# Kernel optimization log

Measured on AMD Instinct MI355X. Metric: run time of the kernel, lower is better.

Reference implementation:

```python
import jax, jax.numpy as jnp
import numpy as np

BS, NS, S = 4, 16384, 8
C_PLANE, RES = 64, 128
IN_DIM = 3 * C_PLANE  # 192


def _bilerp(plane, uv):
    """plane: [B,C,H,W]; uv: [B,n,2] in [0,1] -> [B,n,C] bilinear samples (border clamp)."""
    B, C, H, W = plane.shape
    x = jnp.clip(uv[..., 0], 0.0, 1.0) * (W - 1)
    y = jnp.clip(uv[..., 1], 0.0, 1.0) * (H - 1)
    x0 = jnp.floor(x).astype(jnp.int32)
    y0 = jnp.floor(y).astype(jnp.int32)
    x1 = jnp.minimum(x0 + 1, W - 1)
    y1 = jnp.minimum(y0 + 1, H - 1)
    wx = (x - x0)[:, :, None]
    wy = (y - y0)[:, :, None]
    gat = jax.vmap(lambda p, yy, xx: p[:, yy, xx].T)  # per-batch gather -> [n,C]
    f00 = gat(plane, y0, x0)
    f01 = gat(plane, y0, x1)
    f10 = gat(plane, y1, x0)
    f11 = gat(plane, y1, x1)
    return (f00 * (1 - wx) * (1 - wy) + f01 * wx * (1 - wy)
            + f10 * (1 - wx) * wy + f11 * wx * wy)


def _sample_triplane(p, feat_xz, feat_xy, feat_yz):
    """p: [B,n,3] -> concat of bilinear samples from the three planes: [B,n,3C]."""
    f_xz = _bilerp(feat_xz, p[..., jnp.array([0, 2])])
    f_xy = _bilerp(feat_xy, p[..., jnp.array([0, 1])])
    f_yz = _bilerp(feat_yz, p[..., jnp.array([1, 2])])
    return jnp.concatenate([f_xz, f_xy, f_yz], axis=-1)


def setup_inputs() -> dict:
    key = jax.random.key(0)
    ks = jax.random.split(key, 12)
    w = 0.05  # small init so predicted offsets stay near the query point
    return {
        "query_pos": jax.random.uniform(ks[0], (BS, NS, 3), dtype=jnp.float32),
        "feat_xz": jax.random.normal(ks[1], (BS, C_PLANE, RES, RES), dtype=jnp.float32),
        "feat_xy": jax.random.normal(ks[2], (BS, C_PLANE, RES, RES), dtype=jnp.float32),
        "feat_yz": jax.random.normal(ks[3], (BS, C_PLANE, RES, RES), dtype=jnp.float32),
        "W_v": jax.random.normal(ks[4], (IN_DIM, IN_DIM), dtype=jnp.float32) * w,
        "b_v": jnp.zeros((IN_DIM,), jnp.float32),
        "W_out": jax.random.normal(ks[5], (IN_DIM, IN_DIM), dtype=jnp.float32) * w,
        "b_out": jnp.zeros((IN_DIM,), jnp.float32),
        "W_off": jax.random.normal(ks[6], (3 * S, IN_DIM), dtype=jnp.float32) * w,
        "b_off": jnp.zeros((3 * S,), jnp.float32),
        "W_wt": jax.random.normal(ks[7], (S, IN_DIM), dtype=jnp.float32) * w,
        "b_wt": jnp.zeros((S,), jnp.float32),
    }


def reference(query_pos, feat_xz, feat_xy, feat_yz, W_v, b_v, W_out, b_out,
              W_off, b_off, W_wt, b_wt):
    bs, ns, _ = query_pos.shape
    # feature at query points: [bs, ns, IN_DIM]
    feature = _sample_triplane(query_pos, feat_xz, feat_xy, feat_yz)
    # predicted per-sample offsets and weights
    off = (feature @ W_off.T + b_off).reshape(bs, ns, S, 3)
    wt = (feature @ W_wt.T + b_wt)[..., None]            # [bs, ns, S, 1]
    pts = off + query_pos[:, :, None, :]                  # [bs, ns, S, 3]
    # gather features at offset locations: [bs, ns*S, IN_DIM]
    aux = _sample_triplane(pts.reshape(bs, ns * S, 3), feat_xz, feat_xy, feat_yz)
    v = (aux @ W_v.T + b_v).reshape(bs, ns, S, -1)        # [bs, ns, S, hidden]
    out = (v * wt).sum(axis=-2)                           # weighted sum over samples
    out = out @ W_out.T + b_out + feature                 # residual add
    return out  # [bs, ns, IN_DIM]
```

## Files before the change

kernel.cpp:

```cpp
#include <hip/hip_runtime.h>

#define BS 4
#define NS 16384
#define S_SAMP 8
#define CPL 64
#define RES 128
#define IN_DIM 192
#define NPTS (BS * NS)
#define PL_STRIDE (RES * RES * CPL)
#define PLANES_T_FLOATS (BS * 3 * PL_STRIDE)

__global__ __launch_bounds__(256) void transpose_planes(
    const float* __restrict__ xz, const float* __restrict__ xy,
    const float* __restrict__ yz, float* __restrict__ T) {
  __shared__ float tile[64][33];
  int blk = blockIdx.x;
  int xt = blk & 3;
  int y  = (blk >> 2) & 127;
  int pl = (blk >> 9) % 3;
  int b  = blk / 1536;
  const float* src = (pl == 0) ? xz : ((pl == 1) ? xy : yz);
  src += (size_t)b * CPL * RES * RES + (size_t)y * RES + xt * 32;
  int tid = threadIdx.x;
  int xl = tid & 31, c0 = tid >> 5;
#pragma unroll
  for (int r = 0; r < 8; ++r) {
    int c = c0 + (r << 3);
    tile[c][xl] = src[(size_t)c * RES * RES + xl];
  }
  __syncthreads();
  float* dst = T + ((size_t)(b * 3 + pl) * RES * RES + (size_t)y * RES + xt * 32) * CPL;
  int c2 = tid & 63, x0 = tid >> 6;
#pragma unroll
  for (int r = 0; r < 8; ++r) {
    int xl2 = x0 + (r << 2);
    dst[(size_t)xl2 * CPL + c2] = tile[c2][xl2];
  }
}

__global__ __launch_bounds__(192) void precompute_wc(
    const float* __restrict__ W_v, const float* __restrict__ b_v,
    const float* __restrict__ W_out, float* __restrict__ WcT,
    float* __restrict__ bc) {
  int j = threadIdx.x;
  int k = blockIdx.x;
  if (k < IN_DIM) {
    float acc = 0.f;
    for (int m = 0; m < IN_DIM; ++m)
      acc += W_out[j * IN_DIM + m] * W_v[m * IN_DIM + k];
    WcT[k * IN_DIM + j] = acc;
  } else {
    float acc = 0.f;
    for (int m = 0; m < IN_DIM; ++m)
      acc += W_out[j * IN_DIM + m] * b_v[m];
    bc[j] = acc;
  }
}

__device__ __forceinline__ float bilerp_s(const float* __restrict__ pb, float u,
                                          float v, int lane) {
  u = fminf(fmaxf(u, 0.f), 1.f) * 127.f;
  v = fminf(fmaxf(v, 0.f), 1.f) * 127.f;
  float xf = floorf(u), yf = floorf(v);
  float wx = u - xf, wy = v - yf;
  int x0 = __builtin_amdgcn_readfirstlane((int)xf);
  int y0 = __builtin_amdgcn_readfirstlane((int)yf);
  int dx = (x0 < 127) ? CPL : 0;
  int dy = (y0 < 127) ? RES * CPL : 0;
  const float* b00 = pb + (((y0 << 7) + x0) << 6);
  float f00 = b00[lane];
  float f01 = b00[dx + lane];
  float f10 = b00[dy + lane];
  float f11 = b00[dy + dx + lane];
  float fx0 = f00 + wx * (f01 - f00);
  float fx1 = f10 + wx * (f11 - f10);
  return fx0 + wy * (fx1 - fx0);
}

__global__ __launch_bounds__(256, 4) void fused_sample(
    const float* __restrict__ qpos, const float* __restrict__ planesT,
    const float* __restrict__ W_off, const float* __restrict__ b_off,
    const float* __restrict__ W_wt, const float* __restrict__ b_wt,
    float* __restrict__ waux, float* __restrict__ swtg,
    float* __restrict__ featg) {
  __shared__ float feat_lds[4][IN_DIM];
  __shared__ float offwt[4][32];
  int w = threadIdx.x >> 6, lane = threadIdx.x & 63;
  int p = (blockIdx.x << 2) + w;
  int b = p >> 14;
  float qx = qpos[p * 3 + 0], qy = qpos[p * 3 + 1], qz = qpos[p * 3 + 2];
  const float* Tb = planesT + (size_t)b * 3 * PL_STRIDE;

  float f0 = bilerp_s(Tb, qx, qz, lane);
  float f1 = bilerp_s(Tb + PL_STRIDE, qx, qy, lane);
  float f2 = bilerp_s(Tb + 2 * PL_STRIDE, qy, qz, lane);
  feat_lds[w][lane] = f0;
  feat_lds[w][64 + lane] = f1;
  feat_lds[w][128 + lane] = f2;
  __syncthreads();

  {
    int oj = lane & 31;
    const float* row = (oj < 24) ? (W_off + oj * IN_DIM)
                                 : (W_wt + (oj - 24) * IN_DIM);
    float bias = (oj < 24) ? b_off[oj] : b_wt[oj - 24];
    int k0 = (lane >> 5) * 96;
    const float4* r4 = (const float4*)(row + k0);
    float a0 = 0.f, a1 = 0.f, a2 = 0.f, a3 = 0.f;
#pragma unroll
    for (int k4 = 0; k4 < 24; ++k4) {
      float4 rv = r4[k4];
      a0 += rv.x * feat_lds[w][k0 + 4 * k4 + 0];
      a1 += rv.y * feat_lds[w][k0 + 4 * k4 + 1];
      a2 += rv.z * feat_lds[w][k0 + 4 * k4 + 2];
      a3 += rv.w * feat_lds[w][k0 + 4 * k4 + 3];
    }
    float acc = (a0 + a1) + (a2 + a3);
    acc += __shfl_xor(acc, 32);
    if (lane < 32) offwt[w][oj] = acc + bias;
  }
  __syncthreads();

  float wa0 = 0.f, wa1 = 0.f, wa2 = 0.f, swt = 0.f;
#pragma unroll 4
  for (int s = 0; s < S_SAMP; ++s) {
    float wt = offwt[w][24 + s];
    float px = qx + offwt[w][3 * s + 0];
    float py = qy + offwt[w][3 * s + 1];
    float pz = qz + offwt[w][3 * s + 2];
    wa0 += wt * bilerp_s(Tb, px, pz, lane);
    wa1 += wt * bilerp_s(Tb + PL_STRIDE, px, py, lane);
    wa2 += wt * bilerp_s(Tb + 2 * PL_STRIDE, py, pz, lane);
    swt += wt;
  }

  size_t o = (size_t)p * IN_DIM + lane;
  waux[o] = wa0; waux[o + 64] = wa1; waux[o + 128] = wa2;
  if (lane == 0) swtg[p] = swt;
  featg[o] = f0; featg[o + 64] = f1; featg[o + 128] = f2;
}

__global__ __launch_bounds__(512) void out_gemm(
    const float* __restrict__ waux, const float* __restrict__ swtg,
    const float* __restrict__ WcT, const float* __restrict__ bc,
    const float* __restrict__ b_out, float* __restrict__ out) {
  __shared__ float wtile[64 * IN_DIM];
  int tid = threadIdx.x;
  int w = tid >> 6, lane = tid & 63;
  int p0 = blockIdx.x * 128 + w * 16;

  float acc[4][4][3] = {};
  for (int c = 0; c < 3; ++c) {
#pragma unroll
    for (int r = 0; r < 24; ++r)
      wtile[tid + r * 512] = WcT[c * 64 * IN_DIM + tid + r * 512];
    __syncthreads();
#pragma unroll
    for (int g = 0; g < 4; ++g) {
      const float* wrow[4];
#pragma unroll
      for (int q = 0; q < 4; ++q)
        wrow[q] = waux +
                  (size_t)__builtin_amdgcn_readfirstlane(p0 + g * 4 + q) * IN_DIM +
                  c * 64;
#pragma unroll 4
      for (int k = 0; k < 64; ++k) {
        float v0 = wtile[k * IN_DIM + lane];
        float v1 = wtile[k * IN_DIM + 64 + lane];
        float v2 = wtile[k * IN_DIM + 128 + lane];
#pragma unroll
        for (int q = 0; q < 4; ++q) {
          float wv = wrow[q][k];
          acc[g][q][0] += v0 * wv;
          acc[g][q][1] += v1 * wv;
          acc[g][q][2] += v2 * wv;
        }
      }
    }
    __syncthreads();
  }
#pragma unroll
  for (int g = 0; g < 4; ++g)
#pragma unroll
    for (int q = 0; q < 4; ++q) {
      int p = p0 + g * 4 + q;
      float sw = swtg[p];
#pragma unroll
      for (int t = 0; t < 3; ++t) {
        int j = lane + t * 64;
        size_t o = (size_t)p * IN_DIM + j;
        out[o] = acc[g][q][t] + sw * bc[j] + b_out[j] + out[o];
      }
    }
}

extern "C" void kernel_launch(void* const* d_in, const int* in_sizes, int n_in,
                              void* d_out, int out_size, void* d_ws,
                              size_t ws_size, hipStream_t stream) {
  const float* qpos  = (const float*)d_in[0];
  const float* xz    = (const float*)d_in[1];
  const float* xy    = (const float*)d_in[2];
  const float* yz    = (const float*)d_in[3];
  const float* W_v   = (const float*)d_in[4];
  const float* b_v   = (const float*)d_in[5];
  const float* W_out = (const float*)d_in[6];
  const float* b_out = (const float*)d_in[7];
  const float* W_off = (const float*)d_in[8];
  const float* b_off = (const float*)d_in[9];
  const float* W_wt  = (const float*)d_in[10];
  const float* b_wt  = (const float*)d_in[11];

  float* ws      = (float*)d_ws;
  float* planesT = ws;
  float* waux    = planesT + PLANES_T_FLOATS;
  float* swtg    = waux + (size_t)NPTS * IN_DIM;
  float* WcT     = swtg + NPTS;
  float* bc      = WcT + IN_DIM * IN_DIM;
  float* out     = (float*)d_out;

  hipLaunchKernelGGL(transpose_planes, dim3(BS * 3 * RES * 4), dim3(256), 0,
                     stream, xz, xy, yz, planesT);
  hipLaunchKernelGGL(precompute_wc, dim3(IN_DIM + 1), dim3(IN_DIM), 0, stream,
                     W_v, b_v, W_out, WcT, bc);
  hipLaunchKernelGGL(fused_sample, dim3(NPTS / 4), dim3(256), 0, stream, qpos,
                     planesT, W_off, b_off, W_wt, b_wt, waux, swtg, out);
  hipLaunchKernelGGL(out_gemm, dim3(NPTS / 128), dim3(512), 0, stream, waux,
                     swtg, WcT, bc, b_out, out);
}
```

Measured before the change: 484.6 us.

## Vectorize plane transpose, sampling gathers and restructure output GEMM tiling

Rewrites all four kernels. The plane transpose now moves float4 values in 64-wide tiles. Sampling splits each wave into four lane groups that each handle one sample with float4 channel loads, then reduces across groups with shuffles. The output GEMM stages a 64-point activation tile in LDS and keeps 48 accumulators per thread, reading weights straight from global memory. The goal is wider memory transactions and fewer, larger gathers, at the cost of more register pressure and shuffle reductions.

```diff
diff --git a/kernel.cpp b/kernel.cpp
--- a/kernel.cpp
+++ b/kernel.cpp
@@ -13,28 +13,37 @@
 __global__ __launch_bounds__(256) void transpose_planes(
     const float* __restrict__ xz, const float* __restrict__ xy,
     const float* __restrict__ yz, float* __restrict__ T) {
-  __shared__ float tile[64][33];
+  __shared__ float tile[64][65];
   int blk = blockIdx.x;
-  int xt = blk & 3;
-  int y  = (blk >> 2) & 127;
-  int pl = (blk >> 9) % 3;
-  int b  = blk / 1536;
-  const float* src = (pl == 0) ? xz : ((pl == 1) ? xy : yz);
-  src += (size_t)b * CPL * RES * RES + (size_t)y * RES + xt * 32;
+  int xh = blk & 1;
+  int y  = (blk >> 1) & 127;
+  int pl = (blk >> 8) % 3;
+  int b  = blk / 768;
+  const float* s = ((pl == 0) ? xz : (pl == 1) ? xy : yz) +
+                   (size_t)b * CPL * RES * RES + y * RES + xh * 64;
   int tid = threadIdx.x;
-  int xl = tid & 31, c0 = tid >> 5;
-#pragma unroll
-  for (int r = 0; r < 8; ++r) {
-    int c = c0 + (r << 3);
-    tile[c][xl] = src[(size_t)c * RES * RES + xl];
+  int xi = tid & 15, c0 = tid >> 4;
+#pragma unroll
+  for (int r = 0; r < 4; ++r) {
+    int c = c0 + r * 16;
+    float4 v = *(const float4*)(s + (size_t)c * RES * RES + 4 * xi);
+    tile[c][4 * xi + 0] = v.x;
+    tile[c][4 * xi + 1] = v.y;
+    tile[c][4 * xi + 2] = v.z;
+    tile[c][4 * xi + 3] = v.w;
   }
   __syncthreads();
-  float* dst = T + ((size_t)(b * 3 + pl) * RES * RES + (size_t)y * RES + xt * 32) * CPL;
-  int c2 = tid & 63, x0 = tid >> 6;
-#pragma unroll
-  for (int r = 0; r < 8; ++r) {
-    int xl2 = x0 + (r << 2);
-    dst[(size_t)xl2 * CPL + c2] = tile[c2][xl2];
+  float* d = T + ((size_t)(b * 3 + pl) * RES * RES + (size_t)y * RES + xh * 64) * CPL;
+  int cj = tid & 15, x0 = tid >> 4;
+#pragma unroll
+  for (int r = 0; r < 4; ++r) {
+    int x = x0 + r * 16;
+    float4 v;
+    v.x = tile[4 * cj + 0][x];
+    v.y = tile[4 * cj + 1][x];
+    v.z = tile[4 * cj + 2][x];
+    v.w = tile[4 * cj + 3][x];
+    *(float4*)(d + (size_t)x * CPL + 4 * cj) = v;
   }
 }
 
@@ -42,39 +51,53 @@
     const float* __restrict__ W_v, const float* __restrict__ b_v,
     const float* __restrict__ W_out, float* __restrict__ WcT,
     float* __restrict__ bc) {
-  int j = threadIdx.x;
-  int k = blockIdx.x;
-  if (k < IN_DIM) {
-    float acc = 0.f;
-    for (int m = 0; m < IN_DIM; ++m)
-      acc += W_out[j * IN_DIM + m] * W_v[m * IN_DIM + k];
-    WcT[k * IN_DIM + j] = acc;
+  int j = blockIdx.x;
+  int k = threadIdx.x;
+  if (j < IN_DIM) {
+    float a0 = 0.f, a1 = 0.f, a2 = 0.f, a3 = 0.f;
+#pragma unroll 4
+    for (int m = 0; m < IN_DIM; m += 4) {
+      a0 += W_out[j * IN_DIM + m + 0] * W_v[(m + 0) * IN_DIM + k];
+      a1 += W_out[j * IN_DIM + m + 1] * W_v[(m + 1) * IN_DIM + k];
+      a2 += W_out[j * IN_DIM + m + 2] * W_v[(m + 2) * IN_DIM + k];
+      a3 += W_out[j * IN_DIM + m + 3] * W_v[(m + 3) * IN_DIM + k];
+    }
+    WcT[k * IN_DIM + j] = (a0 + a1) + (a2 + a3);
   } else {
-    float acc = 0.f;
-    for (int m = 0; m < IN_DIM; ++m)
-      acc += W_out[j * IN_DIM + m] * b_v[m];
-    bc[j] = acc;
-  }
-}
-
-__device__ __forceinline__ float bilerp_s(const float* __restrict__ pb, float u,
-                                          float v, int lane) {
-  u = fminf(fmaxf(u, 0.f), 1.f) * 127.f;
-  v = fminf(fmaxf(v, 0.f), 1.f) * 127.f;
-  float xf = floorf(u), yf = floorf(v);
-  float wx = u - xf, wy = v - yf;
-  int x0 = __builtin_amdgcn_readfirstlane((int)xf);
-  int y0 = __builtin_amdgcn_readfirstlane((int)yf);
-  int dx = (x0 < 127) ? CPL : 0;
-  int dy = (y0 < 127) ? RES * CPL : 0;
-  const float* b00 = pb + (((y0 << 7) + x0) << 6);
-  float f00 = b00[lane];
-  float f01 = b00[dx + lane];
-  float f10 = b00[dy + lane];
-  float f11 = b00[dy + dx + lane];
-  float fx0 = f00 + wx * (f01 - f00);
-  float fx1 = f10 + wx * (f11 - f10);
-  return fx0 + wy * (fx1 - fx0);
+    float a0 = 0.f, a1 = 0.f;
+#pragma unroll 4
+    for (int m = 0; m < IN_DIM; m += 2) {
+      a0 += W_out[k * IN_DIM + m] * b_v[m];
+      a1 += W_out[k * IN_DIM + m + 1] * b_v[m + 1];
+    }
+    bc[k] = a0 + a1;
+  }
+}
+
+__device__ __forceinline__ void coordf(float c, int& i, float& fr) {
+  float u = fminf(fmaxf(c, 0.f), 1.f) * 127.f;
+  float uf = floorf(u);
+  i = (int)uf;
+  fr = u - uf;
+}
+
+__device__ __forceinline__ float4 bil4(float4 acc, const float* __restrict__ P,
+                                       unsigned plBase, int iv, int iu,
+                                       float fv, float fu, float wt, int m) {
+  unsigned off = plBase + (unsigned)(iv * RES + iu) * CPL + 4u * m;
+  unsigned du = (iu < 127) ? CPL : 0u;
+  unsigned dv = (iv < 127) ? (unsigned)(RES * CPL) : 0u;
+  float4 t0 = *(const float4*)(P + off);
+  float4 t1 = *(const float4*)(P + off + du);
+  float4 t2 = *(const float4*)(P + off + dv);
+  float4 t3 = *(const float4*)(P + off + dv + du);
+  float a = wt * (1.f - fu), bq = wt * fu;
+  float w0 = a * (1.f - fv), w1 = bq * (1.f - fv), w2 = a * fv, w3 = bq * fv;
+  acc.x += t0.x * w0 + t1.x * w1 + t2.x * w2 + t3.x * w3;
+  acc.y += t0.y * w0 + t1.y * w1 + t2.y * w2 + t3.y * w3;
+  acc.z += t0.z * w0 + t1.z * w1 + t2.z * w2 + t3.z * w3;
+  acc.w += t0.w * w0 + t1.w * w1 + t2.w * w2 + t3.w * w3;
+  return acc;
 }
 
 __global__ __launch_bounds__(256, 4) void fused_sample(
@@ -82,116 +105,153 @@
     const float* __restrict__ W_off, const float* __restrict__ b_off,
     const float* __restrict__ W_wt, const float* __restrict__ b_wt,
     float* __restrict__ waux, float* __restrict__ swtg,
-    float* __restrict__ featg) {
+    float* __restrict__ outp) {
   __shared__ float feat_lds[4][IN_DIM];
   __shared__ float offwt[4][32];
   int w = threadIdx.x >> 6, lane = threadIdx.x & 63;
-  int p = (blockIdx.x << 2) + w;
+  int q = lane >> 4, m = lane & 15;
+  int p = blockIdx.x * 4 + w;
   int b = p >> 14;
   float qx = qpos[p * 3 + 0], qy = qpos[p * 3 + 1], qz = qpos[p * 3 + 2];
-  const float* Tb = planesT + (size_t)b * 3 * PL_STRIDE;
-
-  float f0 = bilerp_s(Tb, qx, qz, lane);
-  float f1 = bilerp_s(Tb + PL_STRIDE, qx, qy, lane);
-  float f2 = bilerp_s(Tb + 2 * PL_STRIDE, qy, qz, lane);
-  feat_lds[w][lane] = f0;
-  feat_lds[w][64 + lane] = f1;
-  feat_lds[w][128 + lane] = f2;
-  __syncthreads();
+  unsigned bOff = (unsigned)b * 3u * PL_STRIDE;
 
   {
-    int oj = lane & 31;
+    int ix, iy, iz;
+    float fx, fy, fz;
+    coordf(qx, ix, fx);
+    coordf(qy, iy, fy);
+    coordf(qz, iz, fz);
+    unsigned off0 = bOff + 0u * PL_STRIDE + (unsigned)(iz * RES + ix) * CPL;
+    unsigned off1 = bOff + 1u * PL_STRIDE + (unsigned)(iy * RES + ix) * CPL;
+    unsigned off2 = bOff + 2u * PL_STRIDE + (unsigned)(iz * RES + iy) * CPL;
+    unsigned du0 = (ix < 127) ? CPL : 0u, dv0 = (iz < 127) ? RES * CPL : 0u;
+    unsigned du1 = (ix < 127) ? CPL : 0u, dv1 = (iy < 127) ? RES * CPL : 0u;
+    unsigned du2 = (iy < 127) ? CPL : 0u, dv2 = (iz < 127) ? RES * CPL : 0u;
+    unsigned offV = (q == 0) ? off0 : (q == 1) ? off1 : off2;
+    unsigned duV = (q == 0) ? du0 : (q == 1) ? du1 : du2;
+    unsigned dvV = (q == 0) ? dv0 : (q == 1) ? dv1 : dv2;
+    float wxV = (q == 0) ? fx : (q == 1) ? fx : fy;
+    float wyV = (q == 0) ? fz : (q == 1) ? fy : fz;
+    offV += 4u * m;
+    float4 t0 = *(const float4*)(planesT + offV);
+    float4 t1 = *(const float4*)(planesT + offV + duV);
+    float4 t2 = *(const float4*)(planesT + offV + dvV);
+    float4 t3 = *(const float4*)(planesT + offV + dvV + duV);
+    float cx = 1.f - wxV, cy = 1.f - wyV;
+    float w0 = cx * cy, w1 = wxV * cy, w2 = cx * wyV, w3 = wxV * wyV;
+    float4 f4;
+    f4.x = t0.x * w0 + t1.x * w1 + t2.x * w2 + t3.x * w3;
+    f4.y = t0.y * w0 + t1.y * w1 + t2.y * w2 + t3.y * w3;
+    f4.z = t0.z * w0 + t1.z * w1 + t2.z * w2 + t3.z * w3;
+    f4.w = t0.w * w0 + t1.w * w1 + t2.w * w2 + t3.w * w3;
+    if (q < 3) {
+      *(float4*)&feat_lds[w][q * 64 + 4 * m] = f4;
+      *(float4*)(outp + (size_t)p * IN_DIM + q * 64 + 4 * m) = f4;
+    }
+  }
+
+  {
+    int oj = lane & 31, kh = lane >> 5;
     const float* row = (oj < 24) ? (W_off + oj * IN_DIM)
                                  : (W_wt + (oj - 24) * IN_DIM);
     float bias = (oj < 24) ? b_off[oj] : b_wt[oj - 24];
-    int k0 = (lane >> 5) * 96;
-    const float4* r4 = (const float4*)(row + k0);
+    const float4* r4 = (const float4*)(row + kh * 96);
+    const float4* fl = (const float4*)&feat_lds[w][kh * 96];
     float a0 = 0.f, a1 = 0.f, a2 = 0.f, a3 = 0.f;
 #pragma unroll
     for (int k4 = 0; k4 < 24; ++k4) {
       float4 rv = r4[k4];
-      a0 += rv.x * feat_lds[w][k0 + 4 * k4 + 0];
-      a1 += rv.y * feat_lds[w][k0 + 4 * k4 + 1];
-      a2 += rv.z * feat_lds[w][k0 + 4 * k4 + 2];
-      a3 += rv.w * feat_lds[w][k0 + 4 * k4 + 3];
+      float4 fv = fl[k4];
+      a0 += rv.x * fv.x;
+      a1 += rv.y * fv.y;
+      a2 += rv.z * fv.z;
+      a3 += rv.w * fv.w;
     }
     float acc = (a0 + a1) + (a2 + a3);
     acc += __shfl_xor(acc, 32);
     if (lane < 32) offwt[w][oj] = acc + bias;
   }
-  __syncthreads();
-
-  float wa0 = 0.f, wa1 = 0.f, wa2 = 0.f, swt = 0.f;
-#pragma unroll 4
-  for (int s = 0; s < S_SAMP; ++s) {
-    float wt = offwt[w][24 + s];
-    float px = qx + offwt[w][3 * s + 0];
-    float py = qy + offwt[w][3 * s + 1];
-    float pz = qz + offwt[w][3 * s + 2];
-    wa0 += wt * bilerp_s(Tb, px, pz, lane);
-    wa1 += wt * bilerp_s(Tb + PL_STRIDE, px, py, lane);
-    wa2 += wt * bilerp_s(Tb + 2 * PL_STRIDE, py, pz, lane);
-    swt += wt;
-  }
-
-  size_t o = (size_t)p * IN_DIM + lane;
-  waux[o] = wa0; waux[o + 64] = wa1; waux[o + 128] = wa2;
-  if (lane == 0) swtg[p] = swt;
-  featg[o] = f0; featg[o + 64] = f1; featg[o + 128] = f2;
-}
-
-__global__ __launch_bounds__(512) void out_gemm(
+
+  float4 acc0 = {0, 0, 0, 0}, acc1 = {0, 0, 0, 0}, acc2 = {0, 0, 0, 0};
+  float swtA = 0.f;
+#pragma unroll
+  for (int sb = 0; sb < 2; ++sb) {
+    int sl = 4 * sb + q;
+    float ox = offwt[w][3 * sl + 0];
+    float oy = offwt[w][3 * sl + 1];
+    float oz = offwt[w][3 * sl + 2];
+    float wt = offwt[w][24 + sl];
+    swtA += wt;
+    int ix, iy, iz;
+    float fx, fy, fz;
+    coordf(qx + ox, ix, fx);
+    coordf(qy + oy, iy, fy);
+    coordf(qz + oz, iz, fz);
+    acc0 = bil4(acc0, planesT, bOff + 0u * PL_STRIDE, iz, ix, fz, fx, wt, m);
+    acc1 = bil4(acc1, planesT, bOff + 1u * PL_STRIDE, iy, ix, fy, fx, wt, m);
+    acc2 = bil4(acc2, planesT, bOff + 2u * PL_STRIDE, iz, iy, fz, fy, wt, m);
+  }
+#define REDQ(v)                          \
+  v.x += __shfl_xor(v.x, 16); v.y += __shfl_xor(v.y, 16); \
+  v.z += __shfl_xor(v.z, 16); v.w += __shfl_xor(v.w, 16); \
+  v.x += __shfl_xor(v.x, 32); v.y += __shfl_xor(v.y, 32); \
+  v.z += __shfl_xor(v.z, 32); v.w += __shfl_xor(v.w, 32);
+  REDQ(acc0)
+  REDQ(acc1)
+  REDQ(acc2)
+#undef REDQ
+  float4 wv = (q == 0) ? acc0 : (q == 1) ? acc1 : acc2;
+  if (q < 3) *(float4*)(waux + (size_t)p * IN_DIM + q * 64 + 4 * m) = wv;
+  swtA += __shfl_xor(swtA, 16);
+  swtA += __shfl_xor(swtA, 32);
+  if (lane == 0) swtg[p] = swtA;
+}
+
+__global__ __launch_bounds__(256) void out_gemm(
     const float* __restrict__ waux, const float* __restrict__ swtg,
     const float* __restrict__ WcT, const float* __restrict__ bc,
     const float* __restrict__ b_out, float* __restrict__ out) {
-  __shared__ float wtile[64 * IN_DIM];
+  __shared__ float at[64][193];
   int tid = threadIdx.x;
   int w = tid >> 6, lane = tid & 63;
-  int p0 = blockIdx.x * 128 + w * 16;
-
-  float acc[4][4][3] = {};
-  for (int c = 0; c < 3; ++c) {
-#pragma unroll
-    for (int r = 0; r < 24; ++r)
-      wtile[tid + r * 512] = WcT[c * 64 * IN_DIM + tid + r * 512];
-    __syncthreads();
-#pragma unroll
-    for (int g = 0; g < 4; ++g) {
-      const float* wrow[4];
-#pragma unroll
-      for (int q = 0; q < 4; ++q)
-        wrow[q] = waux +
-                  (size_t)__builtin_amdgcn_readfirstlane(p0 + g * 4 + q) * IN_DIM +
-                  c * 64;
+  int p0 = blockIdx.x * 64;
+
+  const float4* src = (const float4*)(waux + (size_t)p0 * IN_DIM);
+#pragma unroll
+  for (int i = 0; i < 12; ++i) {
+    int idx = tid + i * 256;
+    int pp = idx / 48, k4 = idx % 48;
+    float4 v = src[idx];
+    at[pp][k4 * 4 + 0] = v.x;
+    at[pp][k4 * 4 + 1] = v.y;
+    at[pp][k4 * 4 + 2] = v.z;
+    at[pp][k4 * 4 + 3] = v.w;
+  }
+  __syncthreads();
+
+  int j0 = __builtin_amdgcn_readfirstlane(w * 48);
+  float acc[48] = {};
 #pragma unroll 4
-      for (int k = 0; k < 64; ++k) {
-        float v0 = wtile[k * IN_DIM + lane];
-        float v1 = wtile[k * IN_DIM + 64 + lane];
-        float v2 = wtile[k * IN_DIM + 128 + lane];
-#pragma unroll
-        for (int q = 0; q < 4; ++q) {
-          float wv = wrow[q][k];
-          acc[g][q][0] += v0 * wv;
-          acc[g][q][1] += v1 * wv;
-          acc[g][q][2] += v2 * wv;
-        }
-      }
-    }
-    __syncthreads();
-  }
-#pragma unroll
-  for (int g = 0; g < 4; ++g)
-#pragma unroll
-    for (int q = 0; q < 4; ++q) {
-      int p = p0 + g * 4 + q;
-      float sw = swtg[p];
-#pragma unroll
-      for (int t = 0; t < 3; ++t) {
-        int j = lane + t * 64;
-        size_t o = (size_t)p * IN_DIM + j;
-        out[o] = acc[g][q][t] + sw * bc[j] + b_out[j] + out[o];
-      }
-    }
+  for (int k = 0; k < 192; ++k) {
+    float a = at[lane][k];
+    const float* wr = WcT + k * IN_DIM + j0;
+#pragma unroll
+    for (int jj = 0; jj < 48; ++jj) acc[jj] += a * wr[jj];
+  }
+
+  int p = p0 + lane;
+  float sw = swtg[p];
+  size_t ob = (size_t)p * IN_DIM + j0;
+#pragma unroll
+  for (int g = 0; g < 12; ++g) {
+    float4 o = *(const float4*)(out + ob + 4 * g);
+    float4 r;
+    r.x = acc[4 * g + 0] + sw * bc[j0 + 4 * g + 0] + b_out[j0 + 4 * g + 0] + o.x;
+    r.y = acc[4 * g + 1] + sw * bc[j0 + 4 * g + 1] + b_out[j0 + 4 * g + 1] + o.y;
+    r.z = acc[4 * g + 2] + sw * bc[j0 + 4 * g + 2] + b_out[j0 + 4 * g + 2] + o.z;
+    r.w = acc[4 * g + 3] + sw * bc[j0 + 4 * g + 3] + b_out[j0 + 4 * g + 3] + o.w;
+    *(float4*)(out + ob + 4 * g) = r;
+  }
 }
 
 extern "C" void kernel_launch(void* const* d_in, const int* in_sizes, int n_in,
@@ -218,12 +278,12 @@
   float* bc      = WcT + IN_DIM * IN_DIM;
   float* out     = (float*)d_out;
 
-  hipLaunchKernelGGL(transpose_planes, dim3(BS * 3 * RES * 4), dim3(256), 0,
+  hipLaunchKernelGGL(transpose_planes, dim3(BS * 3 * RES * 2), dim3(256), 0,
                      stream, xz, xy, yz, planesT);
   hipLaunchKernelGGL(precompute_wc, dim3(IN_DIM + 1), dim3(IN_DIM), 0, stream,
                      W_v, b_v, W_out, WcT, bc);
   hipLaunchKernelGGL(fused_sample, dim3(NPTS / 4), dim3(256), 0, stream, qpos,
                      planesT, W_off, b_off, W_wt, b_wt, waux, swtg, out);
-  hipLaunchKernelGGL(out_gemm, dim3(NPTS / 128), dim3(512), 0, stream, waux,
+  hipLaunchKernelGGL(out_gemm, dim3(NPTS / 64), dim3(256), 0, stream, waux,
                      swtg, WcT, bc, b_out, out);
 }
```

Result: no change. 480.2 us (-0.9%).
